# Performance work log

Measured on AMD Instinct MI355X. Metric: run time of the kernel, lower is better.

The kernel has to match this reference:

```python
import jax, jax.numpy as jnp
import numpy as np

B, T, H, NH = 4, 2048, 2048, 16
HD = H // NH
SCALE = HD ** -0.5

def setup_inputs() -> dict:
    key = jax.random.key(0)
    ks = jax.random.split(key, 9)
    s = H ** -0.5
    return {
        "x": jax.random.normal(ks[0], (B, T, H), jnp.float32),
        "q_w": jax.random.normal(ks[1], (H, H), jnp.float32) * s,
        "q_b": jnp.zeros((H,), jnp.float32),
        "k_w": jax.random.normal(ks[2], (H, H), jnp.float32) * s,
        "k_b": jnp.zeros((H,), jnp.float32),
        "v_w": jax.random.normal(ks[3], (H, H), jnp.float32) * s,
        "v_b": jnp.zeros((H,), jnp.float32),
        "o_w": jax.random.normal(ks[4], (H, H), jnp.float32) * s,
        "o_b": jnp.zeros((H,), jnp.float32),
    }

def reference(x, q_w, q_b, k_w, k_b, v_w, v_b, o_w, o_b):
    Bd, Td, Hd = x.shape
    # projections (torch Linear: y = x @ W^T + b)
    q = (x @ q_w.T + q_b).reshape(Bd, Td, NH, HD).transpose(0, 2, 1, 3)  # [B,nh,T,hd]
    k = (x @ k_w.T + k_b).reshape(Bd, Td, NH, HD).transpose(0, 2, 1, 3)
    v = (x @ v_w.T + v_b).reshape(Bd, Td, NH, HD).transpose(0, 2, 1, 3)
    scores = jnp.einsum('bhqd,bhkd->bhqk', q, k) * SCALE  # [B,nh,T,T]
    causal = jnp.tril(jnp.ones((Td, Td), dtype=bool))
    scores = jnp.where(causal, scores, -jnp.inf)
    probs = jax.nn.softmax(scores, axis=-1)
    ctx = jnp.einsum('bhqk,bhkd->bhqd', probs, v)  # [B,nh,T,hd]
    ctx = ctx.transpose(0, 2, 1, 3).reshape(Bd, Td, Hd)
    return ctx @ o_w.T + o_b
```

## Files before the change

kernel.cpp:

```cpp
#include <hip/hip_runtime.h>
#include <stdint.h>

#define B_SZ 4
#define T_SEQ 2048
#define H_DIM 2048
#define NH_ 16
#define HD_ 128
#define MTOK (B_SZ * T_SEQ)

typedef __attribute__((ext_vector_type(8))) short bf16x8;
typedef __attribute__((ext_vector_type(4))) float f32x4;
typedef __attribute__((ext_vector_type(4))) unsigned short u16x4;

__device__ __forceinline__ unsigned short f2b(float f) {
  union { float f; uint32_t u; } x; x.f = f;
  uint32_t r = x.u + 0x7FFFu + ((x.u >> 16) & 1u);
  return (unsigned short)(r >> 16);
}

__device__ __forceinline__ void gload16(const void* g, void* l) {
  __builtin_amdgcn_global_load_lds((const __attribute__((address_space(1))) void*)g,
                                   (__attribute__((address_space(3))) void*)l, 16, 0, 0);
}

__global__ void cvt_bf16_k(const float* __restrict__ in, unsigned short* __restrict__ out, int n4) {
  for (int i = blockIdx.x * blockDim.x + threadIdx.x; i < n4; i += gridDim.x * blockDim.x) {
    float4 v = ((const float4*)in)[i];
    u16x4 o;
    o[0] = f2b(v.x); o[1] = f2b(v.y); o[2] = f2b(v.z); o[3] = f2b(v.w);
    ((u16x4*)out)[i] = o;
  }
}

template <int MODE>
__global__ __launch_bounds__(512, 2) void gemm256_k(const unsigned short* __restrict__ A,
                                                    const unsigned short* __restrict__ W,
                                                    const float* __restrict__ bias,
                                                    void* __restrict__ outp) {
  constexpr int K = H_DIM;
  constexpr int NT = K / 64;
  __shared__ __align__(16) unsigned short Al[2][256 * 64];
  __shared__ __align__(16) unsigned short Bl[2][256 * 64];

  const int tid = threadIdx.x;
  const int w = tid >> 6, l = tid & 63;
  const int g = l >> 4, ln = l & 15;
  const int wr = w >> 2, wc = w & 3;

  const int bid = blockIdx.x + gridDim.x * blockIdx.y;
  const int fid = ((bid & 7) << 5) | (bid >> 3);
  const int col0 = (fid & 7) * 256;
  const int row0 = (fid >> 3) * 256;

  const char* Ag = (const char*)A;
  const char* Wg = (const char*)W;

  const int srow = l >> 3;
  const int sbyte = ((l & 7) * 16) ^ (srow << 4);

#define ST_A(t2, b2, c)                                                                 \
  gload16(Ag + (((size_t)(row0 + (c) * 8 + srow)) * K + (t2) * 64) * 2 + sbyte,         \
          (char*)&Al[b2][0] + (c) * 1024)
#define ST_B(t2, b2, c)                                                                 \
  gload16(Wg + (((size_t)(col0 + (c) * 8 + srow)) * K + (t2) * 64) * 2 + sbyte,         \
          (char*)&Bl[b2][0] + (c) * 1024)
#define STAGE_A0(t2, b2) do { ST_A(t2, b2, w);  ST_A(t2, b2, 16 + w); } while (0)
#define STAGE_A1(t2, b2) do { ST_A(t2, b2, 8 + w); ST_A(t2, b2, 24 + w); } while (0)
#define STAGE_B0(t2, b2) do { int c_ = (w >> 2) * 8 + (w & 3); ST_B(t2, b2, c_); ST_B(t2, b2, 16 + c_); } while (0)
#define STAGE_B1(t2, b2) do { int c_ = (w >> 2) * 8 + 4 + (w & 3); ST_B(t2, b2, c_); ST_B(t2, b2, 16 + c_); } while (0)

  f32x4 acc[8][4] = {};
  bf16x8 aF[4][2];
  bf16x8 bF[2][2][2];

#define READ_A(mh)                                                                      \
  _Pragma("unroll") for (int mf = 0; mf < 4; ++mf)                                      \
  _Pragma("unroll") for (int ks = 0; ks < 2; ++ks) {                                    \
    int row_ = wr * 128 + (mh) * 64 + mf * 16 + ln;                                     \
    aF[mf][ks] = *(const bf16x8*)((const char*)Ab + row_ * 128 +                        \
                                  ((ks * 64 + g * 16) ^ ((ln & 7) << 4)));              \
  }
#define READ_B(nh)                                                                      \
  _Pragma("unroll") for (int nf = 0; nf < 2; ++nf)                                      \
  _Pragma("unroll") for (int ks = 0; ks < 2; ++ks) {                                    \
    int row_ = wc * 64 + (nh) * 32 + nf * 16 + ln;                                      \
    bF[nh][nf][ks] = *(const bf16x8*)((const char*)Bb + row_ * 128 +                    \
                                      ((ks * 64 + g * 16) ^ ((ln & 7) << 4)));          \
  }
#define MFMA_PHASE(mh, nh)                                                              \
  do {                                                                                  \
    __builtin_amdgcn_s_setprio(1);                                                      \
    _Pragma("unroll") for (int mf = 0; mf < 4; ++mf)                                    \
    _Pragma("unroll") for (int nf = 0; nf < 2; ++nf)                                    \
    _Pragma("unroll") for (int ks = 0; ks < 2; ++ks)                                    \
      acc[(mh) * 4 + mf][(nh) * 2 + nf] = __builtin_amdgcn_mfma_f32_16x16x32_bf16(      \
          aF[mf][ks], bF[nh][nf][ks], acc[(mh) * 4 + mf][(nh) * 2 + nf], 0, 0, 0);      \
    __builtin_amdgcn_s_setprio(0);                                                      \
  } while (0)
#define BARRIER() asm volatile("s_barrier" ::: "memory")

  STAGE_A0(0, 0); STAGE_B0(0, 0); STAGE_B1(0, 0); STAGE_A1(0, 0);
  STAGE_A0(1, 1); STAGE_B0(1, 1); STAGE_B1(1, 1); STAGE_A1(1, 1);
  asm volatile("s_waitcnt vmcnt(8)" ::: "memory");
  BARRIER();

#pragma unroll 1
  for (int t = 0; t < NT; ++t) {
    const int buf = t & 1;
    const unsigned short* Ab = &Al[buf][0];
    const unsigned short* Bb = &Bl[buf][0];
    READ_A(0); READ_B(0);
    if (t >= 1 && t + 1 < NT) STAGE_A1(t + 1, (t + 1) & 1);
    BARRIER();
    MFMA_PHASE(0, 0);
    BARRIER();
    READ_B(1);
    if (t + 2 < NT) STAGE_A0(t + 2, buf);
    BARRIER();
    MFMA_PHASE(0, 1);
    BARRIER();
    READ_A(1);
    if (t + 2 < NT) STAGE_B0(t + 2, buf);
    BARRIER();
    MFMA_PHASE(1, 0);
    BARRIER();
    if (t + 2 < NT) {
      STAGE_B1(t + 2, buf);
      asm volatile("s_waitcnt vmcnt(6)" ::: "memory");
    } else {
      asm volatile("s_waitcnt vmcnt(0)" ::: "memory");
    }
    BARRIER();
    MFMA_PHASE(1, 1);
    BARRIER();
  }

#pragma unroll
  for (int mi = 0; mi < 8; ++mi) {
#pragma unroll
    for (int ni = 0; ni < 4; ++ni) {
      int n = col0 + wc * 64 + ni * 16 + ln;
      float bv = bias[n];
      if constexpr (MODE == 2) {
        float* out = (float*)outp;
#pragma unroll
        for (int r = 0; r < 4; ++r) {
          int m = row0 + wr * 128 + mi * 16 + 4 * g + r;
          out[(size_t)m * H_DIM + n] = acc[mi][ni][r] + bv;
        }
      } else if constexpr (MODE == 0) {
        unsigned short* out = (unsigned short*)outp;
        int h = n >> 7, d = n & 127;
#pragma unroll
        for (int r = 0; r < 4; ++r) {
          int m = row0 + wr * 128 + mi * 16 + 4 * g + r;
          int b = m >> 11, tt = m & 2047;
          out[(((size_t)(b * NH_ + h)) * T_SEQ + tt) * HD_ + d] = f2b(acc[mi][ni][r] + bv);
        }
      } else {
        unsigned short* out = (unsigned short*)outp;
        int h = n >> 7, d = n & 127;
        int m0 = row0 + wr * 128 + mi * 16 + 4 * g;
        int b = m0 >> 11, t0 = m0 & 2047;
        u16x4 pk;
#pragma unroll
        for (int r = 0; r < 4; ++r) pk[r] = f2b(acc[mi][ni][r] + bv);
        *(u16x4*)&out[(((size_t)(b * NH_ + h)) * HD_ + d) * T_SEQ + t0] = pk;
      }
    }
  }
#undef ST_A
#undef ST_B
#undef STAGE_A0
#undef STAGE_A1
#undef STAGE_B0
#undef STAGE_B1
#undef READ_A
#undef READ_B
#undef MFMA_PHASE
#undef BARRIER
}

__global__ __launch_bounds__(512, 2) void attn256_k(const unsigned short* __restrict__ Q,
                                                    const unsigned short* __restrict__ Kg,
                                                    const unsigned short* __restrict__ Vt,
                                                    unsigned short* __restrict__ ctx) {
  __shared__ __align__(16) unsigned short Kl[2][64 * 128];
  __shared__ __align__(16) unsigned short Vl[2][128 * 64];

  const int tid = threadIdx.x;
  const int w = tid >> 6, l = tid & 63;
  const int g = l >> 4, ln = l & 15;

  const int flat = ((blockIdx.x & 7) << 5) | (blockIdx.x >> 3);
  const int qi = flat & 3;
  const int bh = flat >> 2;

  const float cscale = 0.08838834764831845f * 1.4426950408889634f;

  const char* kbase = (const char*)(Kg + (size_t)bh * T_SEQ * HD_);
  const char* vbase = (const char*)(Vt + (size_t)bh * HD_ * T_SEQ);
  const int b = bh >> 4, h = bh & 15;

#define STAGE_KV(bufi, ktile) do {                                                    \
    int kv0_ = (ktile) * 64;                                                          \
    _Pragma("unroll")                                                                 \
    for (int i_ = 0; i_ < 2; ++i_) {                                                  \
      int c_ = w * 2 + i_;                                                            \
      int kvr_ = c_ * 4 + g;                                                          \
      gload16(kbase + ((size_t)(kv0_ + kvr_) * HD_) * 2 + ((ln * 16) ^ ((kvr_ & 7) << 4)), \
              (char*)&Kl[bufi][0] + c_ * 1024);                                       \
      int d_ = c_ * 8 + (l >> 3);                                                     \
      gload16(vbase + ((size_t)d_ * T_SEQ + kv0_) * 2 + (((l & 7) * 16) ^ ((d_ & 7) << 4)), \
              (char*)&Vl[bufi][0] + c_ * 1024);                                       \
    } } while (0)

#pragma unroll 1
  for (int half = 0; half < 2; ++half) {
    const int qt = half ? qi : (7 - qi);
    const int q0 = qt << 8;
    const int qw = q0 + w * 32;

    bf16x8 bq[2][4];
#pragma unroll
    for (int f = 0; f < 2; ++f)
#pragma unroll
      for (int kk = 0; kk < 4; ++kk)
        bq[f][kk] = *(const bf16x8*)(Q + ((size_t)bh * T_SEQ + qw + f * 16 + ln) * HD_ + kk * 32 + g * 8);

    f32x4 acc[2][8] = {};
    float mrun[2] = {-INFINITY, -INFINITY};
    float lrun[2] = {0.f, 0.f};

    const int nt = (qt + 1) * 4;

    STAGE_KV(0, 0);
    __syncthreads();
    int cur = 0;

#pragma unroll 1
    for (int kt = 0; kt < nt; ++kt) {
      if (kt + 1 < nt) STAGE_KV(cur ^ 1, kt + 1);
      const int kv0 = kt * 64;
      if (kv0 <= qw + 31) {
        const char* kl = (const char*)&Kl[cur][0];
        const char* vl = (const char*)&Vl[cur][0];

        f32x4 st[2][4] = {};
        __builtin_amdgcn_s_setprio(1);
#pragma unroll
        for (int kk = 0; kk < 4; ++kk) {
          bf16x8 ak[4];
#pragma unroll
          for (int mf = 0; mf < 4; ++mf)
            ak[mf] = *(const bf16x8*)(kl + (mf * 16 + ln) * 256 + ((kk * 64 + g * 16) ^ ((ln & 7) << 4)));
#pragma unroll
          for (int mf = 0; mf < 4; ++mf) {
            st[0][mf] = __builtin_amdgcn_mfma_f32_16x16x32_bf16(ak[mf], bq[0][kk], st[0][mf], 0, 0, 0);
            st[1][mf] = __builtin_amdgcn_mfma_f32_16x16x32_bf16(ak[mf], bq[1][kk], st[1][mf], 0, 0, 0);
          }
        }
        __builtin_amdgcn_s_setprio(0);

        if (kv0 + 63 > qw) {
#pragma unroll
          for (int f = 0; f < 2; ++f)
#pragma unroll
            for (int mf = 0; mf < 4; ++mf)
#pragma unroll
              for (int r = 0; r < 4; ++r)
                if (kv0 + mf * 16 + g * 4 + r > qw + f * 16 + ln) st[f][mf][r] = -INFINITY;
        }

        bf16x8 ap[2][2];
#pragma unroll
        for (int f = 0; f < 2; ++f) {
          float pmax = -INFINITY;
#pragma unroll
          for (int mf = 0; mf < 4; ++mf)
#pragma unroll
            for (int r = 0; r < 4; ++r) pmax = fmaxf(pmax, st[f][mf][r]);
          pmax = fmaxf(pmax, __shfl_xor(pmax, 16));
          pmax = fmaxf(pmax, __shfl_xor(pmax, 32));
          float tmax = pmax * cscale;
          float msub = mrun[f];
          if (__any(tmax > mrun[f] + 8.f)) {
            msub = fmaxf(mrun[f], tmax);
            float fac = __builtin_amdgcn_exp2f(mrun[f] - msub);
            mrun[f] = msub;
            lrun[f] *= fac;
            float fr[4];
#pragma unroll
            for (int r = 0; r < 4; ++r) fr[r] = __shfl(fac, g * 4 + r);
#pragma unroll
            for (int nf = 0; nf < 8; ++nf) {
              acc[f][nf][0] *= fr[0]; acc[f][nf][1] *= fr[1];
              acc[f][nf][2] *= fr[2]; acc[f][nf][3] *= fr[3];
            }
          }
          uint32_t Aq[4][2];
          float psum = 0.f;
#pragma unroll
          for (int mf = 0; mf < 4; ++mf) {
            float p0 = __builtin_amdgcn_exp2f(st[f][mf][0] * cscale - msub);
            float p1 = __builtin_amdgcn_exp2f(st[f][mf][1] * cscale - msub);
            float p2 = __builtin_amdgcn_exp2f(st[f][mf][2] * cscale - msub);
            float p3 = __builtin_amdgcn_exp2f(st[f][mf][3] * cscale - msub);
            psum += (p0 + p1) + (p2 + p3);
            asm("v_cvt_pk_bf16_f32 %0, %1, %2" : "=v"(Aq[mf][0]) : "v"(p0), "v"(p1));
            asm("v_cvt_pk_bf16_f32 %0, %1, %2" : "=v"(Aq[mf][1]) : "v"(p2), "v"(p3));
          }
          psum += __shfl_xor(psum, 16);
          psum += __shfl_xor(psum, 32);
          lrun[f] += psum;

#pragma unroll
          for (int ks = 0; ks < 2; ++ks) {
            union { uint32_t u[4]; bf16x8 v; } t;
#pragma unroll
            for (int dw = 0; dw < 2; ++dw) {
              uint32_t u0 = (g < 2) ? Aq[2 * ks][dw] : Aq[2 * ks + 1][dw];
              uint32_t w0 = (g < 2) ? Aq[2 * ks + 1][dw] : Aq[2 * ks][dw];
              uint32_t u16v = __shfl_xor(u0, 16);
              uint32_t w32v = __shfl_xor(w0, 32);
              uint32_t w48v = __shfl_xor(w0, 48);
              t.u[dw]     = (g == 0) ? u0   : (g == 1) ? w48v : (g == 2) ? w32v : u16v;
              t.u[2 + dw] = (g == 0) ? u16v : (g == 1) ? w32v : (g == 2) ? w48v : u0;
            }
            ap[f][ks] = t.v;
          }
        }

        __builtin_amdgcn_s_setprio(1);
#pragma unroll
        for (int nf = 0; nf < 8; ++nf) {
          int d = nf * 16 + ln;
#pragma unroll
          for (int ks = 0; ks < 2; ++ks) {
            bf16x8 bv = *(const bf16x8*)(vl + d * 128 + ((ks * 64 + g * 16) ^ ((ln & 7) << 4)));
            acc[0][nf] = __builtin_amdgcn_mfma_f32_16x16x32_bf16(ap[0][ks], bv, acc[0][nf], 0, 0, 0);
            acc[1][nf] = __builtin_amdgcn_mfma_f32_16x16x32_bf16(ap[1][ks], bv, acc[1][nf], 0, 0, 0);
          }
        }
        __builtin_amdgcn_s_setprio(0);
      }
      __syncthreads();
      cur ^= 1;
    }

#pragma unroll
    for (int f = 0; f < 2; ++f) {
      float inv[4];
#pragma unroll
      for (int r = 0; r < 4; ++r) inv[r] = 1.f / __shfl(lrun[f], g * 4 + r);
#pragma unroll
      for (int nf = 0; nf < 8; ++nf) {
#pragma unroll
        for (int r = 0; r < 4; ++r) {
          int qrow = qw + f * 16 + g * 4 + r;
          ctx[((size_t)(b * T_SEQ + qrow)) * H_DIM + h * HD_ + nf * 16 + ln] =
              f2b(acc[f][nf][r] * inv[r]);
        }
      }
    }
  }
#undef STAGE_KV
}

extern "C" void kernel_launch(void* const* d_in, const int* in_sizes, int n_in,
                              void* d_out, int out_size, void* d_ws, size_t ws_size,
                              hipStream_t stream) {
  (void)in_sizes; (void)n_in; (void)out_size; (void)ws_size;
  const float* x  = (const float*)d_in[0];
  const float* qw = (const float*)d_in[1];
  const float* qb = (const float*)d_in[2];
  const float* kw = (const float*)d_in[3];
  const float* kb = (const float*)d_in[4];
  const float* vw = (const float*)d_in[5];
  const float* vb = (const float*)d_in[6];
  const float* ow = (const float*)d_in[7];
  const float* ob = (const float*)d_in[8];

  char* ws = (char*)d_ws;
  unsigned short* xb  = (unsigned short*)(ws);
  unsigned short* qwb = (unsigned short*)(ws + 33554432);
  unsigned short* kwb = (unsigned short*)(ws + 41943040);
  unsigned short* vwb = (unsigned short*)(ws + 50331648);
  unsigned short* owb = (unsigned short*)(ws + 58720256);
  unsigned short* Qb  = (unsigned short*)(ws + 67108864);
  unsigned short* Kb  = (unsigned short*)(ws + 100663296);
  unsigned short* Vtb = (unsigned short*)(ws + 134217728);
  unsigned short* ctxb = xb;

  dim3 blk(256);
  cvt_bf16_k<<<2048, blk, 0, stream>>>(x,  xb,  (MTOK * H_DIM) / 4);
  cvt_bf16_k<<<1024, blk, 0, stream>>>(qw, qwb, (H_DIM * H_DIM) / 4);
  cvt_bf16_k<<<1024, blk, 0, stream>>>(kw, kwb, (H_DIM * H_DIM) / 4);
  cvt_bf16_k<<<1024, blk, 0, stream>>>(vw, vwb, (H_DIM * H_DIM) / 4);
  cvt_bf16_k<<<1024, blk, 0, stream>>>(ow, owb, (H_DIM * H_DIM) / 4);

  dim3 ggrid(H_DIM / 256, MTOK / 256);
  dim3 gblk(512);
  gemm256_k<0><<<ggrid, gblk, 0, stream>>>(xb, qwb, qb, Qb);
  gemm256_k<0><<<ggrid, gblk, 0, stream>>>(xb, kwb, kb, Kb);
  gemm256_k<1><<<ggrid, gblk, 0, stream>>>(xb, vwb, vb, Vtb);

  attn256_k<<<dim3(256), dim3(512), 0, stream>>>(Qb, Kb, Vtb, ctxb);

  gemm256_k<2><<<ggrid, gblk, 0, stream>>>(ctxb, owb, ob, (float*)d_out);
}
```

Measured before the change: 408.5 us.

## Split attention into one block per query tile and fold softmax scale into Q

The attention kernel previously ran 256 blocks, each processing a paired long and short query tile in sequence. It now launches 512 blocks with one query tile each, ordered longest-first, and raises the launch-bounds occupancy hint from 2 to 4 blocks per CU. The softmax scale times log2(e) is folded into the Q projection epilogue, which removes a per-element multiply from the score path. Risks include worse load balance from no longer pairing causal tiles, extra register pressure from the occupancy hint, and a small precision change because Q is scaled before bf16 rounding.

```diff
diff --git a/kernel.cpp b/kernel.cpp
--- a/kernel.cpp
+++ b/kernel.cpp
@@ -36,7 +36,8 @@
 __global__ __launch_bounds__(512, 2) void gemm256_k(const unsigned short* __restrict__ A,
                                                     const unsigned short* __restrict__ W,
                                                     const float* __restrict__ bias,
-                                                    void* __restrict__ outp) {
+                                                    void* __restrict__ outp,
+                                                    float oscale) {
   constexpr int K = H_DIM;
   constexpr int NT = K / 64;
   __shared__ __align__(16) unsigned short Al[2][256 * 64];
@@ -155,7 +156,7 @@
         for (int r = 0; r < 4; ++r) {
           int m = row0 + wr * 128 + mi * 16 + 4 * g + r;
           int b = m >> 11, tt = m & 2047;
-          out[(((size_t)(b * NH_ + h)) * T_SEQ + tt) * HD_ + d] = f2b(acc[mi][ni][r] + bv);
+          out[(((size_t)(b * NH_ + h)) * T_SEQ + tt) * HD_ + d] = f2b((acc[mi][ni][r] + bv) * oscale);
         }
       } else {
         unsigned short* out = (unsigned short*)outp;
@@ -181,7 +182,7 @@
 #undef BARRIER
 }
 
-__global__ __launch_bounds__(512, 2) void attn256_k(const unsigned short* __restrict__ Q,
+__global__ __launch_bounds__(512, 4) void attn256_k(const unsigned short* __restrict__ Q,
                                                     const unsigned short* __restrict__ Kg,
                                                     const unsigned short* __restrict__ Vt,
                                                     unsigned short* __restrict__ ctx) {
@@ -192,11 +193,9 @@
   const int w = tid >> 6, l = tid & 63;
   const int g = l >> 4, ln = l & 15;
 
-  const int flat = ((blockIdx.x & 7) << 5) | (blockIdx.x >> 3);
-  const int qi = flat & 3;
-  const int bh = flat >> 2;
-
-  const float cscale = 0.08838834764831845f * 1.4426950408889634f;
+  const int blk = blockIdx.x;
+  const int qt = 7 - (blk >> 6);
+  const int bh = ((blk & 7) << 3) | ((blk >> 3) & 7);
 
   const char* kbase = (const char*)(Kg + (size_t)bh * T_SEQ * HD_);
   const char* vbase = (const char*)(Vt + (size_t)bh * HD_ * T_SEQ);
@@ -215,152 +214,147 @@
               (char*)&Vl[bufi][0] + c_ * 1024);                                       \
     } } while (0)
 
+  const int q0 = qt << 8;
+  const int qw = q0 + w * 32;
+
+  bf16x8 bq[2][4];
+#pragma unroll
+  for (int f = 0; f < 2; ++f)
+#pragma unroll
+    for (int kk = 0; kk < 4; ++kk)
+      bq[f][kk] = *(const bf16x8*)(Q + ((size_t)bh * T_SEQ + qw + f * 16 + ln) * HD_ + kk * 32 + g * 8);
+
+  f32x4 acc[2][8] = {};
+  float mrun[2] = {-INFINITY, -INFINITY};
+  float lrun[2] = {0.f, 0.f};
+
+  const int nt = (qt + 1) * 4;
+
+  STAGE_KV(0, 0);
+  __syncthreads();
+  int cur = 0;
+
 #pragma unroll 1
-  for (int half = 0; half < 2; ++half) {
-    const int qt = half ? qi : (7 - qi);
-    const int q0 = qt << 8;
-    const int qw = q0 + w * 32;
-
-    bf16x8 bq[2][4];
-#pragma unroll
-    for (int f = 0; f < 2; ++f)
-#pragma unroll
-      for (int kk = 0; kk < 4; ++kk)
-        bq[f][kk] = *(const bf16x8*)(Q + ((size_t)bh * T_SEQ + qw + f * 16 + ln) * HD_ + kk * 32 + g * 8);
-
-    f32x4 acc[2][8] = {};
-    float mrun[2] = {-INFINITY, -INFINITY};
-    float lrun[2] = {0.f, 0.f};
-
-    const int nt = (qt + 1) * 4;
-
-    STAGE_KV(0, 0);
+  for (int kt = 0; kt < nt; ++kt) {
+    if (kt + 1 < nt) STAGE_KV(cur ^ 1, kt + 1);
+    const int kv0 = kt * 64;
+    if (kv0 <= qw + 31) {
+      const char* kl = (const char*)&Kl[cur][0];
+      const char* vl = (const char*)&Vl[cur][0];
+
+      f32x4 st[2][4] = {};
+      __builtin_amdgcn_s_setprio(1);
+#pragma unroll
+      for (int kk = 0; kk < 4; ++kk) {
+        bf16x8 ak[4];
+#pragma unroll
+        for (int mf = 0; mf < 4; ++mf)
+          ak[mf] = *(const bf16x8*)(kl + (mf * 16 + ln) * 256 + ((kk * 64 + g * 16) ^ ((ln & 7) << 4)));
+#pragma unroll
+        for (int mf = 0; mf < 4; ++mf) {
+          st[0][mf] = __builtin_amdgcn_mfma_f32_16x16x32_bf16(ak[mf], bq[0][kk], st[0][mf], 0, 0, 0);
+          st[1][mf] = __builtin_amdgcn_mfma_f32_16x16x32_bf16(ak[mf], bq[1][kk], st[1][mf], 0, 0, 0);
+        }
+      }
+      __builtin_amdgcn_s_setprio(0);
+
+      if (kv0 + 63 > qw) {
+#pragma unroll
+        for (int f = 0; f < 2; ++f)
+#pragma unroll
+          for (int mf = 0; mf < 4; ++mf)
+#pragma unroll
+            for (int r = 0; r < 4; ++r)
+              if (kv0 + mf * 16 + g * 4 + r > qw + f * 16 + ln) st[f][mf][r] = -INFINITY;
+      }
+
+      bf16x8 ap[2][2];
+#pragma unroll
+      for (int f = 0; f < 2; ++f) {
+        float pmax = -INFINITY;
+#pragma unroll
+        for (int mf = 0; mf < 4; ++mf)
+#pragma unroll
+          for (int r = 0; r < 4; ++r) pmax = fmaxf(pmax, st[f][mf][r]);
+        pmax = fmaxf(pmax, __shfl_xor(pmax, 16));
+        pmax = fmaxf(pmax, __shfl_xor(pmax, 32));
+        float msub = mrun[f];
+        if (__any(pmax > mrun[f] + 8.f)) {
+          msub = fmaxf(mrun[f], pmax);
+          float fac = __builtin_amdgcn_exp2f(mrun[f] - msub);
+          mrun[f] = msub;
+          lrun[f] *= fac;
+          float fr[4];
+#pragma unroll
+          for (int r = 0; r < 4; ++r) fr[r] = __shfl(fac, g * 4 + r);
+#pragma unroll
+          for (int nf = 0; nf < 8; ++nf) {
+            acc[f][nf][0] *= fr[0]; acc[f][nf][1] *= fr[1];
+            acc[f][nf][2] *= fr[2]; acc[f][nf][3] *= fr[3];
+          }
+        }
+        uint32_t Aq[4][2];
+        float psum = 0.f;
+#pragma unroll
+        for (int mf = 0; mf < 4; ++mf) {
+          float p0 = __builtin_amdgcn_exp2f(st[f][mf][0] - msub);
+          float p1 = __builtin_amdgcn_exp2f(st[f][mf][1] - msub);
+          float p2 = __builtin_amdgcn_exp2f(st[f][mf][2] - msub);
+          float p3 = __builtin_amdgcn_exp2f(st[f][mf][3] - msub);
+          psum += (p0 + p1) + (p2 + p3);
+          asm("v_cvt_pk_bf16_f32 %0, %1, %2" : "=v"(Aq[mf][0]) : "v"(p0), "v"(p1));
+          asm("v_cvt_pk_bf16_f32 %0, %1, %2" : "=v"(Aq[mf][1]) : "v"(p2), "v"(p3));
+        }
+        psum += __shfl_xor(psum, 16);
+        psum += __shfl_xor(psum, 32);
+        lrun[f] += psum;
+
+#pragma unroll
+        for (int ks = 0; ks < 2; ++ks) {
+          union { uint32_t u[4]; bf16x8 v; } t;
+#pragma unroll
+          for (int dw = 0; dw < 2; ++dw) {
+            uint32_t u0 = (g < 2) ? Aq[2 * ks][dw] : Aq[2 * ks + 1][dw];
+            uint32_t w0 = (g < 2) ? Aq[2 * ks + 1][dw] : Aq[2 * ks][dw];
+            uint32_t u16v = __shfl_xor(u0, 16);
+            uint32_t w32v = __shfl_xor(w0, 32);
+            uint32_t w48v = __shfl_xor(w0, 48);
+            t.u[dw]     = (g == 0) ? u0   : (g == 1) ? w48v : (g == 2) ? w32v : u16v;
+            t.u[2 + dw] = (g == 0) ? u16v : (g == 1) ? w32v : (g == 2) ? w48v : u0;
+          }
+          ap[f][ks] = t.v;
+        }
+      }
+
+      __builtin_amdgcn_s_setprio(1);
+#pragma unroll
+      for (int nf = 0; nf < 8; ++nf) {
+        int d = nf * 16 + ln;
+#pragma unroll
+        for (int ks = 0; ks < 2; ++ks) {
+          bf16x8 bv = *(const bf16x8*)(vl + d * 128 + ((ks * 64 + g * 16) ^ ((ln & 7) << 4)));
+          acc[0][nf] = __builtin_amdgcn_mfma_f32_16x16x32_bf16(ap[0][ks], bv, acc[0][nf], 0, 0, 0);
+          acc[1][nf] = __builtin_amdgcn_mfma_f32_16x16x32_bf16(ap[1][ks], bv, acc[1][nf], 0, 0, 0);
+        }
+      }
+      __builtin_amdgcn_s_setprio(0);
+    }
     __syncthreads();
-    int cur = 0;
-
-#pragma unroll 1
-    for (int kt = 0; kt < nt; ++kt) {
-      if (kt + 1 < nt) STAGE_KV(cur ^ 1, kt + 1);
-      const int kv0 = kt * 64;
-      if (kv0 <= qw + 31) {
-        const char* kl = (const char*)&Kl[cur][0];
-        const char* vl = (const char*)&Vl[cur][0];
-
-        f32x4 st[2][4] = {};
-        __builtin_amdgcn_s_setprio(1);
-#pragma unroll
-        for (int kk = 0; kk < 4; ++kk) {
-          bf16x8 ak[4];
-#pragma unroll
-          for (int mf = 0; mf < 4; ++mf)
-            ak[mf] = *(const bf16x8*)(kl + (mf * 16 + ln) * 256 + ((kk * 64 + g * 16) ^ ((ln & 7) << 4)));
-#pragma unroll
-          for (int mf = 0; mf < 4; ++mf) {
-            st[0][mf] = __builtin_amdgcn_mfma_f32_16x16x32_bf16(ak[mf], bq[0][kk], st[0][mf], 0, 0, 0);
-            st[1][mf] = __builtin_amdgcn_mfma_f32_16x16x32_bf16(ak[mf], bq[1][kk], st[1][mf], 0, 0, 0);
-          }
-        }
-        __builtin_amdgcn_s_setprio(0);
-
-        if (kv0 + 63 > qw) {
-#pragma unroll
-          for (int f = 0; f < 2; ++f)
-#pragma unroll
-            for (int mf = 0; mf < 4; ++mf)
-#pragma unroll
-              for (int r = 0; r < 4; ++r)
-                if (kv0 + mf * 16 + g * 4 + r > qw + f * 16 + ln) st[f][mf][r] = -INFINITY;
-        }
-
-        bf16x8 ap[2][2];
-#pragma unroll
-        for (int f = 0; f < 2; ++f) {
-          float pmax = -INFINITY;
-#pragma unroll
-          for (int mf = 0; mf < 4; ++mf)
-#pragma unroll
-            for (int r = 0; r < 4; ++r) pmax = fmaxf(pmax, st[f][mf][r]);
-          pmax = fmaxf(pmax, __shfl_xor(pmax, 16));
-          pmax = fmaxf(pmax, __shfl_xor(pmax, 32));
-          float tmax = pmax * cscale;
-          float msub = mrun[f];
-          if (__any(tmax > mrun[f] + 8.f)) {
-            msub = fmaxf(mrun[f], tmax);
-            float fac = __builtin_amdgcn_exp2f(mrun[f] - msub);
-            mrun[f] = msub;
-            lrun[f] *= fac;
-            float fr[4];
-#pragma unroll
-            for (int r = 0; r < 4; ++r) fr[r] = __shfl(fac, g * 4 + r);
-#pragma unroll
-            for (int nf = 0; nf < 8; ++nf) {
-              acc[f][nf][0] *= fr[0]; acc[f][nf][1] *= fr[1];
-              acc[f][nf][2] *= fr[2]; acc[f][nf][3] *= fr[3];
-            }
-          }
-          uint32_t Aq[4][2];
-          float psum = 0.f;
-#pragma unroll
-          for (int mf = 0; mf < 4; ++mf) {
-            float p0 = __builtin_amdgcn_exp2f(st[f][mf][0] * cscale - msub);
-            float p1 = __builtin_amdgcn_exp2f(st[f][mf][1] * cscale - msub);
-            float p2 = __builtin_amdgcn_exp2f(st[f][mf][2] * cscale - msub);
-            float p3 = __builtin_amdgcn_exp2f(st[f][mf][3] * cscale - msub);
-            psum += (p0 + p1) + (p2 + p3);
-            asm("v_cvt_pk_bf16_f32 %0, %1, %2" : "=v"(Aq[mf][0]) : "v"(p0), "v"(p1));
-            asm("v_cvt_pk_bf16_f32 %0, %1, %2" : "=v"(Aq[mf][1]) : "v"(p2), "v"(p3));
-          }
-          psum += __shfl_xor(psum, 16);
-          psum += __shfl_xor(psum, 32);
-          lrun[f] += psum;
-
-#pragma unroll
-          for (int ks = 0; ks < 2; ++ks) {
-            union { uint32_t u[4]; bf16x8 v; } t;
-#pragma unroll
-            for (int dw = 0; dw < 2; ++dw) {
-              uint32_t u0 = (g < 2) ? Aq[2 * ks][dw] : Aq[2 * ks + 1][dw];
-              uint32_t w0 = (g < 2) ? Aq[2 * ks + 1][dw] : Aq[2 * ks][dw];
-              uint32_t u16v = __shfl_xor(u0, 16);
-              uint32_t w32v = __shfl_xor(w0, 32);
-              uint32_t w48v = __shfl_xor(w0, 48);
-              t.u[dw]     = (g == 0) ? u0   : (g == 1) ? w48v : (g == 2) ? w32v : u16v;
-              t.u[2 + dw] = (g == 0) ? u16v : (g == 1) ? w32v : (g == 2) ? w48v : u0;
-            }
-            ap[f][ks] = t.v;
-          }
-        }
-
-        __builtin_amdgcn_s_setprio(1);
-#pragma unroll
-        for (int nf = 0; nf < 8; ++nf) {
-          int d = nf * 16 + ln;
-#pragma unroll
-          for (int ks = 0; ks < 2; ++ks) {
-            bf16x8 bv = *(const bf16x8*)(vl + d * 128 + ((ks * 64 + g * 16) ^ ((ln & 7) << 4)));
-            acc[0][nf] = __builtin_amdgcn_mfma_f32_16x16x32_bf16(ap[0][ks], bv, acc[0][nf], 0, 0, 0);
-            acc[1][nf] = __builtin_amdgcn_mfma_f32_16x16x32_bf16(ap[1][ks], bv, acc[1][nf], 0, 0, 0);
-          }
-        }
-        __builtin_amdgcn_s_setprio(0);
-      }
-      __syncthreads();
-      cur ^= 1;
-    }
-
-#pragma unroll
-    for (int f = 0; f < 2; ++f) {
-      float inv[4];
-#pragma unroll
-      for (int r = 0; r < 4; ++r) inv[r] = 1.f / __shfl(lrun[f], g * 4 + r);
-#pragma unroll
-      for (int nf = 0; nf < 8; ++nf) {
-#pragma unroll
-        for (int r = 0; r < 4; ++r) {
-          int qrow = qw + f * 16 + g * 4 + r;
-          ctx[((size_t)(b * T_SEQ + qrow)) * H_DIM + h * HD_ + nf * 16 + ln] =
-              f2b(acc[f][nf][r] * inv[r]);
-        }
+    cur ^= 1;
+  }
+
+#pragma unroll
+  for (int f = 0; f < 2; ++f) {
+    float inv[4];
+#pragma unroll
+    for (int r = 0; r < 4; ++r) inv[r] = 1.f / __shfl(lrun[f], g * 4 + r);
+#pragma unroll
+    for (int nf = 0; nf < 8; ++nf) {
+#pragma unroll
+      for (int r = 0; r < 4; ++r) {
+        int qrow = qw + f * 16 + g * 4 + r;
+        ctx[((size_t)(b * T_SEQ + qrow)) * H_DIM + h * HD_ + nf * 16 + ln] =
+            f2b(acc[f][nf][r] * inv[r]);
       }
     }
   }
@@ -392,6 +386,8 @@
   unsigned short* Vtb = (unsigned short*)(ws + 134217728);
   unsigned short* ctxb = xb;
 
+  const float cscale = 0.08838834764831845f * 1.4426950408889634f;
+
   dim3 blk(256);
   cvt_bf16_k<<<2048, blk, 0, stream>>>(x,  xb,  (MTOK * H_DIM) / 4);
   cvt_bf16_k<<<1024, blk, 0, stream>>>(qw, qwb, (H_DIM * H_DIM) / 4);
@@ -401,11 +397,11 @@
 
   dim3 ggrid(H_DIM / 256, MTOK / 256);
   dim3 gblk(512);
-  gemm256_k<0><<<ggrid, gblk, 0, stream>>>(xb, qwb, qb, Qb);
-  gemm256_k<0><<<ggrid, gblk, 0, stream>>>(xb, kwb, kb, Kb);
-  gemm256_k<1><<<ggrid, gblk, 0, stream>>>(xb, vwb, vb, Vtb);
-
-  attn256_k<<<dim3(256), dim3(512), 0, stream>>>(Qb, Kb, Vtb, ctxb);
-
-  gemm256_k<2><<<ggrid, gblk, 0, stream>>>(ctxb, owb, ob, (float*)d_out);
-}
+  gemm256_k<0><<<ggrid, gblk, 0, stream>>>(xb, qwb, qb, Qb, cscale);
+  gemm256_k<0><<<ggrid, gblk, 0, stream>>>(xb, kwb, kb, Kb, 1.0f);
+  gemm256_k<1><<<ggrid, gblk, 0, stream>>>(xb, vwb, vb, Vtb, 1.0f);
+
+  attn256_k<<<dim3(512), dim3(512), 0, stream>>>(Qb, Kb, Vtb, ctxb);
+
+  gemm256_k<2><<<ggrid, gblk, 0, stream>>>(ctxb, owb, ob, (float*)d_out, 1.0f);
+}
```

Result: slower. 539.9 us (+32.2%).
